# Performance work log

Measured on AMD Instinct MI355X. Metric: run time of the kernel, lower is better.

The kernel has to match this reference:

```python
import jax, jax.numpy as jnp
import numpy as np

N_NODES = 50000
N_EDGES = 800000
N_GRAPHS = 500
D_IN, D_HID, D_OUT = 128, 128, 64


def setup_inputs() -> dict:
    key = jax.random.key(0)
    ks = jax.random.split(key, 8)
    n_feat = jax.random.normal(ks[0], (N_NODES, D_IN), jnp.float32)
    src = jax.random.randint(ks[1], (N_EDGES,), 0, N_NODES, jnp.int32)
    dst = jax.random.randint(ks[2], (N_EDGES,), 0, N_NODES, jnp.int32)
    graph_ids = jnp.sort(jax.random.randint(ks[3], (N_NODES,), 0, N_GRAPHS, jnp.int32))
    W0 = jax.random.normal(ks[4], (D_IN, D_HID), jnp.float32) * 0.05
    b0 = jnp.zeros((D_HID,), jnp.float32)
    W1 = jax.random.normal(ks[5], (D_HID, D_HID), jnp.float32) * 0.05
    b1 = jnp.zeros((D_HID,), jnp.float32)
    W2 = jax.random.normal(ks[6], (D_HID, D_OUT), jnp.float32) * 0.05
    b2 = jnp.zeros((D_OUT,), jnp.float32)
    return dict(n_feat=n_feat, W0=W0, b0=b0, W1=W1, b1=b1, W2=W2, b2=b2,
                src=src, dst=dst, graph_ids=graph_ids)


def _gcn_layer(h, W, b, src, dst, norm_out, norm_in):
    # DGL GraphConv, norm='both': D_out^{-1/2} gather, sum-aggregate at dst,
    # D_in^{-1/2}, then linear transform + bias.
    m = (h * norm_out[:, None])[src]                        # [E, d] gather
    agg = jax.ops.segment_sum(m, dst, num_segments=N_NODES)  # [N, d] scatter-add
    return (agg * norm_in[:, None]) @ W + b


def reference(n_feat, W0, b0, W1, b1, W2, b2, src, dst, graph_ids):
    ones_e = jnp.ones((N_EDGES,), jnp.float32)
    deg_out = jax.ops.segment_sum(ones_e, src, num_segments=N_NODES)
    deg_in = jax.ops.segment_sum(ones_e, dst, num_segments=N_NODES)
    norm_out = jnp.where(deg_out > 0, jax.lax.rsqrt(jnp.maximum(deg_out, 1.0)), 0.0)
    norm_in = jnp.where(deg_in > 0, jax.lax.rsqrt(jnp.maximum(deg_in, 1.0)), 0.0)

    h = jax.nn.relu(_gcn_layer(n_feat, W0, b0, src, dst, norm_out, norm_in))
    h = jax.nn.relu(_gcn_layer(h, W1, b1, src, dst, norm_out, norm_in))
    h = jax.nn.relu(_gcn_layer(h, W2, b2, src, dst, norm_out, norm_in))

    # dgl.mean_nodes: per-graph mean over nodes
    sums = jax.ops.segment_sum(h, graph_ids, num_segments=N_GRAPHS)   # [G, D_OUT]
    counts = jax.ops.segment_sum(jnp.ones((N_NODES,), jnp.float32), graph_ids,
                                 num_segments=N_GRAPHS)
    return sums / jnp.maximum(counts, 1.0)[:, None]
```

## Files before the change

### kernel.cpp

```cpp
#include <hip/hip_runtime.h>
#include <hip/hip_bf16.h>

#define NN 50000
#define NE 800000
#define NG 500

#define NR 8
#define NC 32
#define RNG (NN / NR)
#define CHE (NE / NC)

__device__ __forceinline__ unsigned f2bf(float f) {
    unsigned u = __float_as_uint(f);
    return (u + 0x7fffu + ((u >> 16) & 1u)) >> 16;
}
__device__ __forceinline__ float bf2f(unsigned u16) {
    return __uint_as_float(u16 << 16);
}

__global__ __launch_bounds__(256) void degree_lds_kernel(
        const int* __restrict__ src, const int* __restrict__ dst,
        int* __restrict__ pin, int* __restrict__ pout) {
    __shared__ int hin[RNG], hout[RNG];
    const int tid   = threadIdx.x;
    const int r     = blockIdx.x & (NR - 1);
    const int c     = blockIdx.x / NR;
    const int rbase = r * RNG;
    for (int i = tid; i < RNG; i += 256) { hin[i] = 0; hout[i] = 0; }
    __syncthreads();
    const int4* s4 = (const int4*)(src + c * CHE);
    const int4* d4 = (const int4*)(dst + c * CHE);
    for (int i = tid; i < CHE / 4; i += 256) {
        int4 s = s4[i];
        int4 d = d4[i];
        unsigned a;
        a = (unsigned)(d.x - rbase); if (a < RNG) atomicAdd(&hin[a], 1);
        a = (unsigned)(d.y - rbase); if (a < RNG) atomicAdd(&hin[a], 1);
        a = (unsigned)(d.z - rbase); if (a < RNG) atomicAdd(&hin[a], 1);
        a = (unsigned)(d.w - rbase); if (a < RNG) atomicAdd(&hin[a], 1);
        a = (unsigned)(s.x - rbase); if (a < RNG) atomicAdd(&hout[a], 1);
        a = (unsigned)(s.y - rbase); if (a < RNG) atomicAdd(&hout[a], 1);
        a = (unsigned)(s.z - rbase); if (a < RNG) atomicAdd(&hout[a], 1);
        a = (unsigned)(s.w - rbase); if (a < RNG) atomicAdd(&hout[a], 1);
    }
    __syncthreads();
    for (int i = tid; i < RNG; i += 256) {
        pin [c * NN + rbase + i] = hin[i];
        pout[c * NN + rbase + i] = hout[i];
    }
}

__global__ void reduce_norms_kernel(const int* __restrict__ pin, const int* __restrict__ pout,
                                    int* __restrict__ deg_in_tot,
                                    float* __restrict__ norm_in,
                                    float* __restrict__ norm_out, int n) {
    int i = blockIdx.x * blockDim.x + threadIdx.x;
    if (i >= n) return;
    int di = 0, dq = 0;
    #pragma unroll
    for (int c = 0; c < NC; c++) {
        di += pin [c * NN + i];
        dq += pout[c * NN + i];
    }
    deg_in_tot[i] = di;
    norm_in[i]  = di > 0 ? 1.0f / sqrtf((float)di) : 0.f;
    norm_out[i] = dq > 0 ? 1.0f / sqrtf((float)dq) : 0.f;
}

__global__ void scan_degrees4(const int* __restrict__ deg, int* __restrict__ row_ptr,
                              int* __restrict__ cursor, int n) {
    __shared__ int wsum[16];
    __shared__ int carry_s, ctot_s;
    const int tid = threadIdx.x, lane = tid & 63, wv = tid >> 6;
    if (tid == 0) { carry_s = 0; row_ptr[0] = 0; }
    __syncthreads();
    for (int base = 0; base < n; base += 4096) {
        const int i0 = base + tid * 4;
        int v0 = 0, v1 = 0, v2 = 0, v3 = 0;
        if (i0 + 3 < n) {
            int4 v = *(const int4*)(deg + i0);
            v0 = v.x; v1 = v.y; v2 = v.z; v3 = v.w;
        } else if (i0 < n) {
            v0 = deg[i0];
            if (i0 + 1 < n) v1 = deg[i0 + 1];
            if (i0 + 2 < n) v2 = deg[i0 + 2];
        }
        const int l0 = v0, l1 = l0 + v1, l2 = l1 + v2, l3 = l2 + v3;
        int x = l3;
        #pragma unroll
        for (int off = 1; off < 64; off <<= 1) {
            int y = __shfl_up(x, off);
            if (lane >= off) x += y;
        }
        if (lane == 63) wsum[wv] = x;
        __syncthreads();
        if (wv == 0) {
            int t = (lane < 16) ? wsum[lane] : 0;
            int s = t;
            #pragma unroll
            for (int off = 1; off < 16; off <<= 1) {
                int y = __shfl_up(s, off);
                if (lane >= off) s += y;
            }
            if (lane < 16) wsum[lane] = s - t;
            if (lane == 15) ctot_s = s;
        }
        __syncthreads();
        const int pre = carry_s + wsum[wv] + (x - l3);
        if (i0 < n)     { cursor[i0]     = pre;      row_ptr[i0 + 1] = pre + l0; }
        if (i0 + 1 < n) { cursor[i0 + 1] = pre + l0; row_ptr[i0 + 2] = pre + l1; }
        if (i0 + 2 < n) { cursor[i0 + 2] = pre + l1; row_ptr[i0 + 3] = pre + l2; }
        if (i0 + 3 < n) { cursor[i0 + 3] = pre + l2; row_ptr[i0 + 4] = pre + l3; }
        __syncthreads();
        if (tid == 0) carry_s += ctot_s;
        __syncthreads();
    }
}

__global__ void place_kernel(const int* __restrict__ src, const int* __restrict__ dst,
                             int* __restrict__ cursor, int* __restrict__ esrc, int E) {
    int e = blockIdx.x * blockDim.x + threadIdx.x;
    if (e < E) {
        int p = atomicAdd(&cursor[dst[e]], 1);
        esrc[p] = src[e];
    }
}

template<int DO, int ROWS>
__global__ __launch_bounds__(256) void gemm_reg_bf(
        const float* __restrict__ A, const float* __restrict__ W,
        const float* __restrict__ norm, unsigned short* __restrict__ out, int nrows) {
    constexpr int DI  = 128;
    constexpr int KC  = 32;
    constexpr int CXN = DO / 8;
    constexpr int RYN = 256 / CXN;
    static_assert(ROWS == RYN * 8, "tile mismatch");
    __shared__ float At[KC][ROWS + 4];
    __shared__ float Wl[KC][DO + 4];

    const int tid  = threadIdx.x;
    const int cx   = tid % CXN;
    const int ry   = tid / CXN;
    const int row0 = blockIdx.x * ROWS;

    float acc[8][8] = {};

    for (int kc = 0; kc < DI; kc += KC) {
        __syncthreads();
        constexpr int AF4 = ROWS * KC / 4;
        #pragma unroll
        for (int i = tid; i < AF4; i += 256) {
            int r  = i >> 3;
            int kq = i & 7;
            float4 v = make_float4(0.f, 0.f, 0.f, 0.f);
            int gr = row0 + r;
            if (gr < nrows) {
                v = ((const float4*)(A + (size_t)gr * DI + kc))[kq];
                float s = norm[gr];
                v.x *= s; v.y *= s; v.z *= s; v.w *= s;
            }
            At[kq * 4 + 0][r] = v.x;
            At[kq * 4 + 1][r] = v.y;
            At[kq * 4 + 2][r] = v.z;
            At[kq * 4 + 3][r] = v.w;
        }
        constexpr int WF4 = KC * DO / 4;
        #pragma unroll
        for (int i = tid; i < WF4; i += 256) {
            int k  = i / (DO / 4);
            int c4 = i % (DO / 4);
            *(float4*)&Wl[k][c4 * 4] = ((const float4*)(W + (size_t)(kc + k) * DO))[c4];
        }
        __syncthreads();
        #pragma unroll 4
        for (int k = 0; k < KC; k++) {
            float a[8], w[8];
            *(float4*)&a[0] = *(const float4*)&At[k][ry * 4];
            *(float4*)&a[4] = *(const float4*)&At[k][ROWS / 2 + ry * 4];
            *(float4*)&w[0] = *(const float4*)&Wl[k][cx * 4];
            *(float4*)&w[4] = *(const float4*)&Wl[k][DO / 2 + cx * 4];
            #pragma unroll
            for (int i = 0; i < 8; i++)
                #pragma unroll
                for (int j = 0; j < 8; j++)
                    acc[i][j] += a[i] * w[j];
        }
    }
    #pragma unroll
    for (int i = 0; i < 8; i++) {
        int r  = (i < 4) ? (ry * 4 + i) : (ROWS / 2 + ry * 4 + (i - 4));
        int gr = row0 + r;
        if (gr < nrows) {
            unsigned short* orow = out + (size_t)gr * DO;
            uint2 lo, hi;
            lo.x = f2bf(acc[i][0]) | (f2bf(acc[i][1]) << 16);
            lo.y = f2bf(acc[i][2]) | (f2bf(acc[i][3]) << 16);
            hi.x = f2bf(acc[i][4]) | (f2bf(acc[i][5]) << 16);
            hi.y = f2bf(acc[i][6]) | (f2bf(acc[i][7]) << 16);
            ((uint2*)orow)[cx]            = lo;
            ((uint2*)(orow + DO / 2))[cx] = hi;
        }
    }
}

template<int D>
__global__ __launch_bounds__(256) void aggregate_bf(
        const unsigned short* __restrict__ t, const int* __restrict__ row_ptr,
        const int* __restrict__ esrc, const float* __restrict__ norm_in,
        const float* __restrict__ bias, float* __restrict__ out, int n) {
    const int wid  = (blockIdx.x * blockDim.x + threadIdx.x) >> 6;
    const int lane = threadIdx.x & 63;
    if (wid >= n) return;
    const int beg = row_ptr[wid], end = row_ptr[wid + 1];
    if (D == 128) {
        const unsigned* tp = (const unsigned*)t;
        float ax0 = 0, ay0 = 0, ax1 = 0, ay1 = 0, ax2 = 0, ay2 = 0, ax3 = 0, ay3 = 0;
        int e = beg;
        for (; e + 3 < end; e += 4) {
            int s0 = esrc[e], s1 = esrc[e + 1], s2 = esrc[e + 2], s3 = esrc[e + 3];
            unsigned v0 = tp[(size_t)s0 * 64 + lane];
            unsigned v1 = tp[(size_t)s1 * 64 + lane];
            unsigned v2 = tp[(size_t)s2 * 64 + lane];
            unsigned v3 = tp[(size_t)s3 * 64 + lane];
            ax0 += bf2f(v0 & 0xffffu); ay0 += bf2f(v0 >> 16);
            ax1 += bf2f(v1 & 0xffffu); ay1 += bf2f(v1 >> 16);
            ax2 += bf2f(v2 & 0xffffu); ay2 += bf2f(v2 >> 16);
            ax3 += bf2f(v3 & 0xffffu); ay3 += bf2f(v3 >> 16);
        }
        for (; e < end; e++) {
            unsigned v = tp[(size_t)esrc[e] * 64 + lane];
            ax0 += bf2f(v & 0xffffu); ay0 += bf2f(v >> 16);
        }
        float ni = norm_in[wid];
        float2 bb = ((const float2*)bias)[lane];
        float2 o;
        o.x = fmaxf((ax0 + ax1 + ax2 + ax3) * ni + bb.x, 0.f);
        o.y = fmaxf((ay0 + ay1 + ay2 + ay3) * ni + bb.y, 0.f);
        ((float2*)out)[(size_t)wid * 64 + lane] = o;
    } else {
        float a0 = 0, a1 = 0, a2 = 0, a3 = 0;
        int e = beg;
        for (; e + 3 < end; e += 4) {
            int s0 = esrc[e], s1 = esrc[e + 1], s2 = esrc[e + 2], s3 = esrc[e + 3];
            a0 += bf2f(t[(size_t)s0 * 64 + lane]);
            a1 += bf2f(t[(size_t)s1 * 64 + lane]);
            a2 += bf2f(t[(size_t)s2 * 64 + lane]);
            a3 += bf2f(t[(size_t)s3 * 64 + lane]);
        }
        for (; e < end; e++) a0 += bf2f(t[(size_t)esrc[e] * 64 + lane]);
        float o = fmaxf((a0 + a1 + a2 + a3) * norm_in[wid] + bias[lane], 0.f);
        out[(size_t)wid * 64 + lane] = o;
    }
}

__global__ __launch_bounds__(256) void readout_partial(
        const float* __restrict__ h, const int* __restrict__ gids,
        float* __restrict__ sums, float* __restrict__ counts, int n) {
    const int wid  = (blockIdx.x * blockDim.x + threadIdx.x) >> 6;
    const int lane = threadIdx.x & 63;
    const int beg = wid * 64;
    if (beg >= n) return;
    const int end = min(beg + 64, n);
    int cur = gids[beg];
    float acc = 0.f; int cnt = 0;
    for (int i = beg; i < end; i++) {
        int g = gids[i];
        if (g != cur) {
            atomicAdd(&sums[(size_t)cur * 64 + lane], acc);
            if (lane == 0) atomicAdd(&counts[cur], (float)cnt);
            cur = g; acc = 0.f; cnt = 0;
        }
        acc += h[(size_t)i * 64 + lane];
        cnt++;
    }
    atomicAdd(&sums[(size_t)cur * 64 + lane], acc);
    if (lane == 0) atomicAdd(&counts[cur], (float)cnt);
}

__global__ void finalize_kernel(const float* __restrict__ sums, const float* __restrict__ counts,
                                float* __restrict__ out, int total) {
    int i = blockIdx.x * blockDim.x + threadIdx.x;
    if (i < total) out[i] = sums[i] / fmaxf(counts[i >> 6], 1.f);
}

extern "C" void kernel_launch(void* const* d_in, const int* in_sizes, int n_in,
                              void* d_out, int out_size, void* d_ws, size_t ws_size,
                              hipStream_t stream) {
    const float* n_feat = (const float*)d_in[0];
    const float* W0 = (const float*)d_in[1];
    const float* b0 = (const float*)d_in[2];
    const float* W1 = (const float*)d_in[3];
    const float* b1 = (const float*)d_in[4];
    const float* W2 = (const float*)d_in[5];
    const float* b2 = (const float*)d_in[6];
    const int* src  = (const int*)d_in[7];
    const int* dst  = (const int*)d_in[8];
    const int* gids = (const int*)d_in[9];
    float* out = (float*)d_out;

    char* ws = (char*)d_ws;
    int*            esrc       = (int*)   (ws + 0);
    float*          norm_out   = (float*) (ws + 3200000);
    float*          norm_in    = (float*) (ws + 3400000);
    int*            deg_in_tot = (int*)   (ws + 3600000);
    int*            row_ptr    = (int*)   (ws + 3800000);
    int*            cursor     = (int*)   (ws + 4000064);
    float*          sums       = (float*) (ws + 4200064);
    float*          counts     = (float*) (ws + 4328064);
    unsigned short* bufA       = (unsigned short*)(ws + 4330112);
    float*          bufB       = (float*) (ws + 29930112);
    int*            pin        = (int*)   (ws + 4330112);
    int*            pout       = (int*)   (ws + 4330112 + 6400000);

    hipMemsetAsync(sums, 0, (NG * 64 + NG) * sizeof(float), stream);

    degree_lds_kernel<<<NR * NC, 256, 0, stream>>>(src, dst, pin, pout);
    reduce_norms_kernel<<<(NN + 255) / 256, 256, 0, stream>>>(pin, pout, deg_in_tot,
                                                              norm_in, norm_out, NN);
    scan_degrees4<<<1, 1024, 0, stream>>>(deg_in_tot, row_ptr, cursor, NN);
    place_kernel<<<(NE + 255) / 256, 256, 0, stream>>>(src, dst, cursor, esrc, NE);

    const int g128 = (NN + 127) / 128;
    const int g64  = (NN + 255) / 256;
    const int agg_grid = (NN + 3) / 4;

    gemm_reg_bf<128, 128><<<g128, 256, 0, stream>>>(n_feat, W0, norm_out, bufA, NN);
    aggregate_bf<128><<<agg_grid, 256, 0, stream>>>(bufA, row_ptr, esrc, norm_in, b0, bufB, NN);
    gemm_reg_bf<128, 128><<<g128, 256, 0, stream>>>(bufB, W1, norm_out, bufA, NN);
    aggregate_bf<128><<<agg_grid, 256, 0, stream>>>(bufA, row_ptr, esrc, norm_in, b1, bufB, NN);
    gemm_reg_bf<64, 256><<<g64, 256, 0, stream>>>(bufB, W2, norm_out, bufA, NN);
    aggregate_bf<64><<<agg_grid, 256, 0, stream>>>(bufA, row_ptr, esrc, norm_in, b2, bufB, NN);

    const int ro_threads = ((NN + 63) / 64) * 64;
    readout_partial<<<(ro_threads + 255) / 256, 256, 0, stream>>>(bufB, gids, sums, counts, NN);
    finalize_kernel<<<(NG * 64 + 255) / 256, 256, 0, stream>>>(sums, counts, out, NG * 64);
}
```

Before: 431.0 us.

## Replace global-atomic edge placement with per-chunk LDS cursors

Swaps the CSR placement kernel, which did one global atomicAdd per edge, for a two-step scheme. The first step computes a per-(edge chunk, node range) start offset from the per-chunk degree histograms. The second places edges using LDS atomics on those cursors. This targets global atomic contention and serialization during CSR construction. It adds a 6.4MB offsets buffer and a kernel where each block scans its whole edge chunk but keeps only the edges whose destination falls in its node range.

```diff
diff --git a/kernel.cpp b/kernel.cpp
--- a/kernel.cpp
+++ b/kernel.cpp
@@ -117,12 +117,39 @@
     }
 }
 
-__global__ void place_kernel(const int* __restrict__ src, const int* __restrict__ dst,
-                             int* __restrict__ cursor, int* __restrict__ esrc, int E) {
-    int e = blockIdx.x * blockDim.x + threadIdx.x;
-    if (e < E) {
-        int p = atomicAdd(&cursor[dst[e]], 1);
-        esrc[p] = src[e];
+__global__ void chunk_offsets_kernel(const int* __restrict__ pin,
+                                     const int* __restrict__ row_ptr,
+                                     int* __restrict__ pcur, int n) {
+    int i = blockIdx.x * blockDim.x + threadIdx.x;
+    if (i >= n) return;
+    int off = row_ptr[i];
+    #pragma unroll
+    for (int c = 0; c < NC; c++) {
+        pcur[c * NN + i] = off;
+        off += pin[c * NN + i];
+    }
+}
+
+__global__ __launch_bounds__(256) void place_lds_kernel(
+        const int* __restrict__ src, const int* __restrict__ dst,
+        const int* __restrict__ pcur, int* __restrict__ esrc) {
+    __shared__ int lcur[RNG];
+    const int tid   = threadIdx.x;
+    const int r     = blockIdx.x & (NR - 1);
+    const int c     = blockIdx.x / NR;
+    const int rbase = r * RNG;
+    for (int i = tid; i < RNG; i += 256) lcur[i] = pcur[c * NN + rbase + i];
+    __syncthreads();
+    const int4* s4 = (const int4*)(src + c * CHE);
+    const int4* d4 = (const int4*)(dst + c * CHE);
+    for (int i = tid; i < CHE / 4; i += 256) {
+        int4 s = s4[i];
+        int4 d = d4[i];
+        unsigned a;
+        a = (unsigned)(d.x - rbase); if (a < RNG) esrc[atomicAdd(&lcur[a], 1)] = s.x;
+        a = (unsigned)(d.y - rbase); if (a < RNG) esrc[atomicAdd(&lcur[a], 1)] = s.y;
+        a = (unsigned)(d.z - rbase); if (a < RNG) esrc[atomicAdd(&lcur[a], 1)] = s.z;
+        a = (unsigned)(d.w - rbase); if (a < RNG) esrc[atomicAdd(&lcur[a], 1)] = s.w;
     }
 }
 
@@ -308,9 +335,10 @@
     float*          sums       = (float*) (ws + 4200064);
     float*          counts     = (float*) (ws + 4328064);
     unsigned short* bufA       = (unsigned short*)(ws + 4330112);
-    float*          bufB       = (float*) (ws + 29930112);
     int*            pin        = (int*)   (ws + 4330112);
     int*            pout       = (int*)   (ws + 4330112 + 6400000);
+    int*            pcur       = (int*)   (ws + 17200000);
+    float*          bufB       = (float*) (ws + 29930112);
 
     hipMemsetAsync(sums, 0, (NG * 64 + NG) * sizeof(float), stream);
 
@@ -318,7 +346,8 @@
     reduce_norms_kernel<<<(NN + 255) / 256, 256, 0, stream>>>(pin, pout, deg_in_tot,
                                                               norm_in, norm_out, NN);
     scan_degrees4<<<1, 1024, 0, stream>>>(deg_in_tot, row_ptr, cursor, NN);
-    place_kernel<<<(NE + 255) / 256, 256, 0, stream>>>(src, dst, cursor, esrc, NE);
+    chunk_offsets_kernel<<<(NN + 255) / 256, 256, 0, stream>>>(pin, row_ptr, pcur, NN);
+    place_lds_kernel<<<NR * NC, 256, 0, stream>>>(src, dst, pcur, esrc);
 
     const int g128 = (NN + 127) / 128;
     const int g64  = (NN + 255) / 256;
```

Result: faster. 410.2 us (-4.8%).
